# Optimization experiments

Hardware: AMD Instinct MI355X
Metric: run time of the kernel (lower is better)

## Reference

```python
import jax, jax.numpy as jnp
import numpy as np

# ---- model hyperparameters (match init_kwargs) ----
THRESHOLD = 1.0
DECAY = 0.9
RESET = 0.0
BATCH = 256
INPUT_DIM = 1024
HIDDEN_DIM = 2048
OUTPUT_DIM = 10
NUM_LAYERS = 2
SIM_STEPS = 100
SPIKE_PROB = 0.2  # density of input spike bins


def setup_inputs() -> dict:
    key = jax.random.key(0)
    k1, k2, k3, k4 = jax.random.split(key, 4)
    # binary spike bins: [B, input_dim, T]
    input_bins = (jax.random.uniform(k1, (BATCH, INPUT_DIM, SIM_STEPS)) < SPIKE_PROB).astype(jnp.float32)
    W_ih = jax.random.normal(k2, (INPUT_DIM, HIDDEN_DIM), dtype=jnp.float32) * 0.1
    W_hh = jax.random.normal(k3, (NUM_LAYERS - 1, HIDDEN_DIM, HIDDEN_DIM), dtype=jnp.float32) * 0.1
    W_ho = jax.random.normal(k4, (HIDDEN_DIM, OUTPUT_DIM), dtype=jnp.float32) * 0.1
    return {"input_bins": input_bins, "W_ih": W_ih, "W_hh": W_hh, "W_ho": W_ho}


def _lif_step(v, current):
    """One leaky-integrate-and-fire update. v, current: [B, N]."""
    v = v * DECAY + current
    spiked = v >= THRESHOLD
    spikes = jnp.where(spiked, 1.0, 0.0).astype(v.dtype)
    v = jnp.where(spiked, RESET, v)
    return v, spikes


def reference(input_bins, W_ih, W_hh, W_ho):
    B = input_bins.shape[0]
    T = input_bins.shape[2]
    x = jnp.transpose(input_bins, (2, 0, 1))  # [T, B, input_dim]
    v_hidden = tuple(jnp.zeros((B, W_ih.shape[1]), input_bins.dtype) for _ in range(NUM_LAYERS))
    v_out = jnp.zeros((B, W_ho.shape[1]), input_bins.dtype)

    def step(carry, inp_t):
        vs, vo = carry
        vs = list(vs)
        vs[0], s = _lif_step(vs[0], inp_t @ W_ih)
        for i in range(NUM_LAYERS - 1):
            vs[i + 1], s = _lif_step(vs[i + 1], s @ W_hh[i])
        # modulator signal is 0 here -> output_input * (1 + 0*0.1) = output_input
        vo, s_out = _lif_step(vo, s @ W_ho)
        return (tuple(vs), vo), s_out

    _, out_spikes = jax.lax.scan(step, (v_hidden, v_out), x)  # [T, B, output_dim]
    output_rates = out_spikes.sum(axis=0) / T  # [B, output_dim]
    return output_rates
```

## Files before the change

kernel.cpp:

```cpp
#include <hip/hip_runtime.h>
#include <hip/hip_bf16.h>


#define B 256
#define IN_DIM 1024
#define HID 2048
#define OUT_DIM 10
#define T_STEPS 100
#define NCH 4
#define RT (T_STEPS * B)

typedef unsigned long long ull;
typedef int v4i __attribute__((ext_vector_type(4)));

template<int K>
__global__ __launch_bounds__(256) void cvt_w_i8(
    const float* __restrict__ W, signed char* __restrict__ Bq)
{
    constexpr int WPR = K / 64;
    size_t id = (size_t)blockIdx.x * 256 + threadIdx.x;
    if (id >= (size_t)(K / 4) * HID) return;
    int n  = (int)(id % HID);
    int kg = (int)(id / HID);
    int k0 = kg * 4;
    signed char dig[4][4];
#pragma unroll
    for (int i = 0; i < 4; ++i) {
        double w = (double)W[(size_t)(k0 + i) * HID + n];
        long long V = __double2ll_rn(w * 2147483648.0);
#pragma unroll
        for (int c = 0; c < 3; ++c) {
            int r = (int)(signed char)(V & 0xFF);
            dig[c][i] = (signed char)r;
            V = (V - r) >> 8;
        }
        dig[3][i] = (signed char)V;
    }
    int wb = k0 >> 6, lk = (k0 >> 4) & 3, jj = k0 & 15;
    int nb32 = n >> 5, ct = (n >> 4) & 1, li = n & 15;
    int lane = lk * 16 + li;
    size_t base = ((size_t)nb32 * WPR + wb) * 8192 + (size_t)lane * 16 + jj;
#pragma unroll
    for (int c = 0; c < 4; ++c) {
        int pc = (c < 3) ? (c * 2 + ct) : (6 + ct);
        unsigned pk = (unsigned)(unsigned char)dig[c][0]
                    | ((unsigned)(unsigned char)dig[c][1] << 8)
                    | ((unsigned)(unsigned char)dig[c][2] << 16)
                    | ((unsigned)(unsigned char)dig[c][3] << 24);
        *reinterpret_cast<unsigned*>(Bq + base + (size_t)pc * 1024) = pk;
    }
}

__global__ __launch_bounds__(256) void cvt_who(
    const float* __restrict__ who, double* __restrict__ Who64)
{
    int i = blockIdx.x * 256 + threadIdx.x;
    if (i < HID * OUT_DIM) Who64[i] = (double)who[i];
}

__global__ __launch_bounds__(256) void bitpack_input(
    const float* __restrict__ inp, ull* __restrict__ XbitsT)
{
    int g = blockIdx.x * 4 + (threadIdx.x >> 6);
    int lane = threadIdx.x & 63;
    int b = g >> 4;
    int ig = g & 15;
    int i = ig * 64 + lane;
    const float4* p = (const float4*)(inp + ((size_t)b * IN_DIM + i) * T_STEPS);
    ull* dst = XbitsT + (size_t)ig * RT + b;
#pragma unroll 1
    for (int t4 = 0; t4 < T_STEPS / 4; ++t4) {
        float4 v = p[t4];
        ull m0 = __ballot(v.x > 0.5f);
        ull m1 = __ballot(v.y > 0.5f);
        ull m2 = __ballot(v.z > 0.5f);
        ull m3 = __ballot(v.w > 0.5f);
        if (lane == 0) {
            dst[(size_t)(t4 * 4 + 0) * B] = m0;
            dst[(size_t)(t4 * 4 + 1) * B] = m1;
            dst[(size_t)(t4 * 4 + 2) * B] = m2;
            dst[(size_t)(t4 * 4 + 3) * B] = m3;
        }
    }
}

template<int K>
__global__ __launch_bounds__(256, 3) void gemm_i8(
    const ull* __restrict__ bitsT, int row_base,
    const signed char* __restrict__ Bq, float* __restrict__ C)
{
    constexpr int WPR = K / 64;
    constexpr int NP  = WPR / 2;
    __shared__ __align__(16) signed char blds[6][8192];

    const int tid = threadIdx.x;
    const int lane = tid & 63;
    const int wv = __builtin_amdgcn_readfirstlane(tid >> 6);
    const int row0 = blockIdx.x * 128;
    const int c0 = blockIdx.y * 32;
    const int li = lane & 15;
    const int lk = lane >> 4;
    const int sh = lk * 16;
    const int r0l = wv * 32;

    const signed char* __restrict__ bsrc = Bq + (size_t)blockIdx.y * WPR * 8192;
    const ull* __restrict__ m0p = bitsT + (row_base + row0 + r0l + li);
    const ull* __restrict__ m1p = m0p + 16;

    auto stage_b = [&](int w, int slot) {
        const signed char* src = bsrc + (size_t)w * 8192 + lane * 16;
        signed char* db = &blds[0][0] + slot * 8192;
        __builtin_amdgcn_global_load_lds(
            (const __attribute__((address_space(1))) unsigned int*)(src + wv * 1024),
            (__attribute__((address_space(3))) unsigned int*)(db + wv * 1024), 16, 0, 0);
        __builtin_amdgcn_global_load_lds(
            (const __attribute__((address_space(1))) unsigned int*)(src + (wv + 4) * 1024),
            (__attribute__((address_space(3))) unsigned int*)(db + (wv + 4) * 1024), 16, 0, 0);
    };

    stage_b(0, 0);
    stage_b(1, 1);
    stage_b(2, 2);
    stage_b(3, 3);
    ull r0[4], r1[4];
#pragma unroll
    for (int u = 0; u < 4; ++u) {
        r0[u] = m0p[(size_t)u * RT];
        r1[u] = m1p[(size_t)u * RT];
    }
    __syncthreads();

    v4i acc[2][2][NCH];
#pragma unroll
    for (int g = 0; g < 2; ++g)
#pragma unroll
        for (int t = 0; t < 2; ++t)
#pragma unroll
            for (int c = 0; c < NCH; ++c) acc[g][t][c] = (v4i){0, 0, 0, 0};

    int s0 = 0;
#pragma unroll 1
    for (int p2 = 0; p2 < NP; p2 += 2) {
#pragma unroll
        for (int pp = 0; pp < 2; ++pp) {
            const int w0 = (p2 + pp) * 2;
            const int u0 = w0 & 3, u1 = (w0 + 1) & 3;
            int s1 = s0 + 1; if (s1 >= 6) s1 -= 6;
            int t0 = s0 + 4; if (t0 >= 6) t0 -= 6;
            int t1 = s0 + 5; if (t1 >= 6) t1 -= 6;

            int wn0 = w0 + 4; if (wn0 >= WPR) wn0 -= WPR;
            int wn1 = w0 + 5; if (wn1 >= WPR) wn1 -= WPR;
            stage_b(wn0, t0);
            stage_b(wn1, t1);
            ull m00 = r0[u0], m01 = r1[u0];
            ull m10 = r0[u1], m11 = r1[u1];
            r0[u0] = m0p[(size_t)wn0 * RT];
            r1[u0] = m1p[(size_t)wn0 * RT];
            r0[u1] = m0p[(size_t)wn1 * RT];
            r1[u1] = m1p[(size_t)wn1 * RT];

            {
                unsigned sa = (unsigned)(m00 >> sh) & 0xFFFFu;
                unsigned sb = (unsigned)(m01 >> sh) & 0xFFFFu;
                v4i a0, a1;
#pragma unroll
                for (int d = 0; d < 4; ++d) {
                    a0[d] = (int)((((sa >> (4 * d)) & 0xFu) * 0x00204081u) & 0x01010101u);
                    a1[d] = (int)((((sb >> (4 * d)) & 0xFu) * 0x00204081u) & 0x01010101u);
                }
                const signed char* bb = &blds[0][0] + s0 * 8192 + lane * 16;
                __builtin_amdgcn_s_setprio(1);
#pragma unroll
                for (int c = 0; c < NCH; ++c) {
#pragma unroll
                    for (int t = 0; t < 2; ++t) {
                        v4i b = *(const v4i*)(bb + (c * 2 + t) * 1024);
                        acc[0][t][c] = __builtin_amdgcn_mfma_i32_16x16x64_i8(a0, b, acc[0][t][c], 0, 0, 0);
                        acc[1][t][c] = __builtin_amdgcn_mfma_i32_16x16x64_i8(a1, b, acc[1][t][c], 0, 0, 0);
                    }
                }
                __builtin_amdgcn_s_setprio(0);
            }
            {
                unsigned sa = (unsigned)(m10 >> sh) & 0xFFFFu;
                unsigned sb = (unsigned)(m11 >> sh) & 0xFFFFu;
                v4i a0, a1;
#pragma unroll
                for (int d = 0; d < 4; ++d) {
                    a0[d] = (int)((((sa >> (4 * d)) & 0xFu) * 0x00204081u) & 0x01010101u);
                    a1[d] = (int)((((sb >> (4 * d)) & 0xFu) * 0x00204081u) & 0x01010101u);
                }
                const signed char* bb = &blds[0][0] + s1 * 8192 + lane * 16;
                __builtin_amdgcn_s_setprio(1);
#pragma unroll
                for (int c = 0; c < NCH; ++c) {
#pragma unroll
                    for (int t = 0; t < 2; ++t) {
                        v4i b = *(const v4i*)(bb + (c * 2 + t) * 1024);
                        acc[0][t][c] = __builtin_amdgcn_mfma_i32_16x16x64_i8(a0, b, acc[0][t][c], 0, 0, 0);
                        acc[1][t][c] = __builtin_amdgcn_mfma_i32_16x16x64_i8(a1, b, acc[1][t][c], 0, 0, 0);
                    }
                }
                __builtin_amdgcn_s_setprio(0);
            }

            __asm__ __volatile__("s_waitcnt vmcnt(8)\n\ts_barrier" ::: "memory");
            s0 += 2; if (s0 >= 6) s0 -= 6;
        }
    }

#pragma unroll
    for (int g = 0; g < 2; ++g) {
#pragma unroll
        for (int t = 0; t < 2; ++t) {
#pragma unroll
            for (int r = 0; r < 4; ++r) {
                long long V = (long long)acc[g][t][3][r];
                V = (V << 8) + (long long)acc[g][t][2][r];
                V = (V << 8) + (long long)acc[g][t][1][r];
                V = (V << 8) + (long long)acc[g][t][0][r];
                C[(size_t)(row0 + r0l + g * 16 + lk * 4 + r) * HID + c0 + t * 16 + li] =
                    (float)((double)V * 0x1p-31);
            }
        }
    }
}

__global__ __launch_bounds__(256) void gemm_out(
    const ull* __restrict__ bitsT, int row_base,
    const double* __restrict__ W, double* __restrict__ C3)
{
    __shared__ double part[3][64][OUT_DIM];
    const int lane = threadIdx.x & 63;
    const int sl = threadIdx.x >> 6;
    const int row = blockIdx.x * 64 + lane;

    double acc[OUT_DIM];
#pragma unroll
    for (int j = 0; j < OUT_DIM; ++j) acc[j] = 0.0;

    for (int w = sl * 8; w < sl * 8 + 8; ++w) {
        ull m = bitsT[(size_t)w * RT + row_base + row];
        const double* __restrict__ wk = W + (size_t)(w * 64) * OUT_DIM;
#pragma unroll 4
        for (int kk = 0; kk < 64; ++kk) {
            double bd = (double)(unsigned int)(m & 1ull);
            m >>= 1;
#pragma unroll
            for (int j = 0; j < OUT_DIM; ++j)
                acc[j] = fma(bd, wk[j], acc[j]);
            wk += OUT_DIM;
        }
    }
    if (sl) {
#pragma unroll
        for (int j = 0; j < OUT_DIM; ++j) part[sl - 1][lane][j] = acc[j];
    }
    __syncthreads();
    if (sl == 0) {
        double* __restrict__ crow = C3 + (size_t)row * OUT_DIM;
#pragma unroll
        for (int j = 0; j < OUT_DIM; ++j)
            crow[j] = acc[j] + part[0][lane][j] + part[1][lane][j] + part[2][lane][j];
    }
}

__global__ __launch_bounds__(256) void lif_scan(
    const float* __restrict__ C, double* __restrict__ vstate,
    ull* __restrict__ SbitsT, int row_base, int Tl, int first)
{
    int g = blockIdx.x * 4 + (threadIdx.x >> 6);
    int lane = threadIdx.x & 63;
    int b = g >> 5;
    int ng = g & 31;
    int n = ng * 64 + lane;
    const float* __restrict__ Cp = C + (size_t)b * HID + n;
    ull* __restrict__ Sp = SbitsT + (size_t)ng * RT + row_base + b;
    double v = first ? 0.0 : vstate[(size_t)b * HID + n];
    int tl = 0;
    for (; tl + 4 <= Tl; tl += 4) {
        float c0 = Cp[(size_t)(tl + 0) * (B * HID)];
        float c1 = Cp[(size_t)(tl + 1) * (B * HID)];
        float c2 = Cp[(size_t)(tl + 2) * (B * HID)];
        float c3 = Cp[(size_t)(tl + 3) * (B * HID)];
#pragma unroll
        for (int i = 0; i < 4; ++i) {
            float cc = (i == 0) ? c0 : (i == 1) ? c1 : (i == 2) ? c2 : c3;
            v = v * 0.9 + (double)cc;
            bool s = (v >= 1.0);
            if (s) v = 0.0;
            ull mask = __ballot(s);
            if (lane == 0) Sp[(size_t)(tl + i) * B] = mask;
        }
    }
    for (; tl < Tl; ++tl) {
        double c = (double)Cp[(size_t)tl * (B * HID)];
        v = v * 0.9 + c;
        bool s = (v >= 1.0);
        if (s) v = 0.0;
        ull mask = __ballot(s);
        if (lane == 0) Sp[(size_t)tl * B] = mask;
    }
    vstate[(size_t)b * HID + n] = v;
}

__global__ __launch_bounds__(256) void lif_out(
    const double* __restrict__ C3, double* __restrict__ vstate,
    int* __restrict__ cnt_state, float* __restrict__ out, int Tl, int first)
{
    int tid = blockIdx.x * 256 + threadIdx.x;
    if (tid >= B * OUT_DIM) return;
    int b = tid / OUT_DIM, o = tid % OUT_DIM;
    const double* __restrict__ Cp = C3 + (size_t)b * OUT_DIM + o;
    double v = first ? 0.0 : vstate[tid];
    int cnt = first ? 0 : cnt_state[tid];
    int tl = 0;
    for (; tl + 4 <= Tl; tl += 4) {
        double c0 = Cp[(size_t)(tl + 0) * (B * OUT_DIM)];
        double c1 = Cp[(size_t)(tl + 1) * (B * OUT_DIM)];
        double c2 = Cp[(size_t)(tl + 2) * (B * OUT_DIM)];
        double c3 = Cp[(size_t)(tl + 3) * (B * OUT_DIM)];
#pragma unroll
        for (int i = 0; i < 4; ++i) {
            double cc = (i == 0) ? c0 : (i == 1) ? c1 : (i == 2) ? c2 : c3;
            v = v * 0.9 + cc;
            if (v >= 1.0) { cnt++; v = 0.0; }
        }
    }
    for (; tl < Tl; ++tl) {
        double c = Cp[(size_t)tl * (B * OUT_DIM)];
        v = v * 0.9 + c;
        if (v >= 1.0) { cnt++; v = 0.0; }
    }
    vstate[tid] = v;
    cnt_state[tid] = cnt;
    out[tid] = (float)((double)cnt / (double)T_STEPS);
}

extern "C" void kernel_launch(void* const* d_in, const int* in_sizes, int n_in,
                              void* d_out, int out_size, void* d_ws, size_t ws_size,
                              hipStream_t stream) {
    const float* inp = (const float*)d_in[0];
    const float* wih = (const float*)d_in[1];
    const float* whh = (const float*)d_in[2];
    const float* who = (const float*)d_in[3];
    float* out = (float*)d_out;

    unsigned char* p = (unsigned char*)d_ws;
    auto alloc = [&](size_t sz) -> void* {
        void* r = (void*)p;
        p += (sz + 255) & ~(size_t)255;
        return r;
    };
    signed char* Bq1 = (signed char*)alloc((size_t)NCH * HID * IN_DIM + 4096);
    signed char* Bq2 = (signed char*)alloc((size_t)NCH * HID * HID + 4096);
    double* Who64 = (double*)alloc((size_t)HID * OUT_DIM * 8);
    ull* XbitsT = (ull*)alloc((size_t)16 * RT * 8);
    ull* S1T    = (ull*)alloc((size_t)32 * RT * 8);
    ull* S2T    = (ull*)alloc((size_t)32 * RT * 8);
    double* v1 = (double*)alloc((size_t)B * HID * 8);
    double* v2 = (double*)alloc((size_t)B * HID * 8);
    double* vo = (double*)alloc((size_t)B * OUT_DIM * 8);
    int* cnts  = (int*)alloc((size_t)B * OUT_DIM * 4);

    size_t used = (size_t)(p - (unsigned char*)d_ws);
    size_t remain = (ws_size > used) ? (ws_size - used) : 0;
    size_t per_t = (size_t)B * HID * 4 + (size_t)B * OUT_DIM * 8 + 1024;
    int CH = (int)(remain / per_t);
    if (CH > T_STEPS) CH = T_STEPS;
    if (CH < 1) CH = 1;
    double* C3 = (double*)alloc((size_t)CH * B * OUT_DIM * 8);
    float* C   = (float*)alloc((size_t)CH * B * HID * 4);

    cvt_w_i8<IN_DIM><<<((IN_DIM / 4) * HID + 255) / 256, 256, 0, stream>>>(wih, Bq1);
    cvt_w_i8<HID><<<((HID / 4) * HID + 255) / 256, 256, 0, stream>>>(whh, Bq2);
    cvt_who<<<(HID * OUT_DIM + 255) / 256, 256, 0, stream>>>(who, Who64);
    bitpack_input<<<(B * (IN_DIM / 64)) / 4, 256, 0, stream>>>(inp, XbitsT);

    for (int t0 = 0; t0 < T_STEPS; t0 += CH) {
        int L = T_STEPS - t0;
        if (L > CH) L = CH;
        int rows = L * B;
        int first = (t0 == 0) ? 1 : 0;

        gemm_i8<IN_DIM><<<dim3(rows / 128, HID / 32), 256, 0, stream>>>(
            XbitsT, t0 * B, Bq1, C);
        lif_scan<<<(B * (HID / 64)) / 4, 256, 0, stream>>>(
            C, v1, S1T, t0 * B, L, first);

        gemm_i8<HID><<<dim3(rows / 128, HID / 32), 256, 0, stream>>>(
            S1T, t0 * B, Bq2, C);
        lif_scan<<<(B * (HID / 64)) / 4, 256, 0, stream>>>(
            C, v2, S2T, t0 * B, L, first);

        gemm_out<<<rows / 64, 256, 0, stream>>>(S2T, t0 * B, Who64, C3);
        lif_out<<<(B * OUT_DIM + 255) / 256, 256, 0, stream>>>(
            C3, vo, cnts, out, L, first);
    }
}
```

Baseline: 999.0 us.

## Move output projection to int8 MFMA and stage input bitpacking through LDS

Replaces the fp64 FMA loop in the output-layer GEMM with int8 MFMA over 4 byte-planes of fixed-point weights, using a new weight-conversion kernel. The input bitpacking kernel now loads through shared memory in coalesced chunks instead of strided float4 reads per lane. The gemm_i8 wait count changes from 8 to 12, and the weight-plane layout formula is simplified. The changes aim to cut the scalar fp64 cost and uncoalesced input loads. They rely on the same fixed-point decomposition for exactness, and the looser vmcnt could affect the pipeline's correctness margin.

```diff
diff --git a/kernel.cpp b/kernel.cpp
--- a/kernel.cpp
+++ b/kernel.cpp
@@ -42,7 +42,7 @@
     size_t base = ((size_t)nb32 * WPR + wb) * 8192 + (size_t)lane * 16 + jj;
 #pragma unroll
     for (int c = 0; c < 4; ++c) {
-        int pc = (c < 3) ? (c * 2 + ct) : (6 + ct);
+        int pc = c * 2 + ct;
         unsigned pk = (unsigned)(unsigned char)dig[c][0]
                     | ((unsigned)(unsigned char)dig[c][1] << 8)
                     | ((unsigned)(unsigned char)dig[c][2] << 16)
@@ -51,36 +51,79 @@
     }
 }
 
-__global__ __launch_bounds__(256) void cvt_who(
-    const float* __restrict__ who, double* __restrict__ Who64)
-{
-    int i = blockIdx.x * 256 + threadIdx.x;
-    if (i < HID * OUT_DIM) Who64[i] = (double)who[i];
+__global__ __launch_bounds__(256) void cvt_who_i8(
+    const float* __restrict__ who, signed char* __restrict__ Bq3)
+{
+    int id = blockIdx.x * 256 + threadIdx.x;
+    if (id >= 32 * 64 * 4) return;
+    int jg = id & 3;
+    int lane = (id >> 2) & 63;
+    int w = id >> 8;
+    int li = lane & 15, lk = lane >> 4;
+    signed char dig[4][4];
+#pragma unroll
+    for (int i = 0; i < 4; ++i) {
+        int jj = jg * 4 + i;
+        int k = w * 64 + lk * 16 + jj;
+        double x = (li < OUT_DIM) ? (double)who[(size_t)k * OUT_DIM + li] : 0.0;
+        long long V = __double2ll_rn(x * 2147483648.0);
+#pragma unroll
+        for (int c = 0; c < 3; ++c) {
+            int r = (int)(signed char)(V & 0xFF);
+            dig[c][i] = (signed char)r;
+            V = (V - r) >> 8;
+        }
+        dig[3][i] = (signed char)V;
+    }
+    size_t base = (size_t)w * 4096 + (size_t)lane * 16 + jg * 4;
+#pragma unroll
+    for (int c = 0; c < 4; ++c) {
+        unsigned pk = (unsigned)(unsigned char)dig[c][0]
+                    | ((unsigned)(unsigned char)dig[c][1] << 8)
+                    | ((unsigned)(unsigned char)dig[c][2] << 16)
+                    | ((unsigned)(unsigned char)dig[c][3] << 24);
+        *reinterpret_cast<unsigned*>(Bq3 + base + (size_t)c * 1024) = pk;
+    }
 }
 
 __global__ __launch_bounds__(256) void bitpack_input(
     const float* __restrict__ inp, ull* __restrict__ XbitsT)
 {
-    int g = blockIdx.x * 4 + (threadIdx.x >> 6);
-    int lane = threadIdx.x & 63;
-    int b = g >> 4;
-    int ig = g & 15;
-    int i = ig * 64 + lane;
-    const float4* p = (const float4*)(inp + ((size_t)b * IN_DIM + i) * T_STEPS);
-    ull* dst = XbitsT + (size_t)ig * RT + b;
-#pragma unroll 1
-    for (int t4 = 0; t4 < T_STEPS / 4; ++t4) {
-        float4 v = p[t4];
-        ull m0 = __ballot(v.x > 0.5f);
-        ull m1 = __ballot(v.y > 0.5f);
-        ull m2 = __ballot(v.z > 0.5f);
-        ull m3 = __ballot(v.w > 0.5f);
-        if (lane == 0) {
-            dst[(size_t)(t4 * 4 + 0) * B] = m0;
-            dst[(size_t)(t4 * 4 + 1) * B] = m1;
-            dst[(size_t)(t4 * 4 + 2) * B] = m2;
-            dst[(size_t)(t4 * 4 + 3) * B] = m3;
-        }
+    __shared__ float sb[4][64][33];
+    const int wv = threadIdx.x >> 6;
+    const int lane = threadIdx.x & 63;
+    const int g = blockIdx.x * 4 + wv;
+    const int b = g >> 4;
+    const int ig = g & 15;
+    const float* __restrict__ src = inp + ((size_t)b * IN_DIM + ig * 64) * T_STEPS;
+    ull* __restrict__ dst = XbitsT + (size_t)ig * RT + b;
+
+#pragma unroll
+    for (int tc = 0; tc < 4; ++tc) {
+        const int t0 = tc * 32;
+        if (tc < 3) {
+#pragma unroll
+            for (int f4 = 0; f4 < 32; ++f4) {
+                int f = f4 * 64 + lane;
+                int ii = f >> 5, tt = f & 31;
+                sb[wv][ii][tt] = src[ii * T_STEPS + t0 + tt];
+            }
+        } else {
+#pragma unroll
+            for (int f4 = 0; f4 < 4; ++f4) {
+                int f = f4 * 64 + lane;
+                int ii = f >> 2, tt = f & 3;
+                sb[wv][ii][tt] = src[ii * T_STEPS + t0 + tt];
+            }
+        }
+        __syncthreads();
+        const int len = (tc < 3) ? 32 : 4;
+        for (int tt = 0; tt < len; ++tt) {
+            float v = sb[wv][lane][tt];
+            ull m = __ballot(v > 0.5f);
+            if (lane == 0) dst[(size_t)(t0 + tt) * B] = m;
+        }
+        __syncthreads();
     }
 }
 
@@ -205,7 +248,7 @@
                 __builtin_amdgcn_s_setprio(0);
             }
 
-            __asm__ __volatile__("s_waitcnt vmcnt(8)\n\ts_barrier" ::: "memory");
+            __asm__ __volatile__("s_waitcnt vmcnt(12)\n\ts_barrier" ::: "memory");
             s0 += 2; if (s0 >= 6) s0 -= 6;
         }
     }
@@ -229,40 +272,57 @@
 
 __global__ __launch_bounds__(256) void gemm_out(
     const ull* __restrict__ bitsT, int row_base,
-    const double* __restrict__ W, double* __restrict__ C3)
-{
-    __shared__ double part[3][64][OUT_DIM];
+    const signed char* __restrict__ Bq3, double* __restrict__ C3)
+{
     const int lane = threadIdx.x & 63;
-    const int sl = threadIdx.x >> 6;
-    const int row = blockIdx.x * 64 + lane;
-
-    double acc[OUT_DIM];
-#pragma unroll
-    for (int j = 0; j < OUT_DIM; ++j) acc[j] = 0.0;
-
-    for (int w = sl * 8; w < sl * 8 + 8; ++w) {
-        ull m = bitsT[(size_t)w * RT + row_base + row];
-        const double* __restrict__ wk = W + (size_t)(w * 64) * OUT_DIM;
-#pragma unroll 4
-        for (int kk = 0; kk < 64; ++kk) {
-            double bd = (double)(unsigned int)(m & 1ull);
-            m >>= 1;
-#pragma unroll
-            for (int j = 0; j < OUT_DIM; ++j)
-                acc[j] = fma(bd, wk[j], acc[j]);
-            wk += OUT_DIM;
-        }
-    }
-    if (sl) {
-#pragma unroll
-        for (int j = 0; j < OUT_DIM; ++j) part[sl - 1][lane][j] = acc[j];
-    }
-    __syncthreads();
-    if (sl == 0) {
-        double* __restrict__ crow = C3 + (size_t)row * OUT_DIM;
-#pragma unroll
-        for (int j = 0; j < OUT_DIM; ++j)
-            crow[j] = acc[j] + part[0][lane][j] + part[1][lane][j] + part[2][lane][j];
+    const int wv = threadIdx.x >> 6;
+    const int li = lane & 15;
+    const int lk = lane >> 4;
+    const int sh = lk * 16;
+    const int row0 = blockIdx.x * 256 + wv * 64;
+    const ull* __restrict__ mp = bitsT + (row_base + row0 + li);
+
+    v4i acc[4][NCH];
+#pragma unroll
+    for (int g = 0; g < 4; ++g)
+#pragma unroll
+        for (int c = 0; c < NCH; ++c) acc[g][c] = (v4i){0, 0, 0, 0};
+
+#pragma unroll 1
+    for (int w = 0; w < 32; ++w) {
+        ull m[4];
+#pragma unroll
+        for (int g = 0; g < 4; ++g) m[g] = mp[(size_t)w * RT + g * 16];
+        const v4i* __restrict__ bp = (const v4i*)(Bq3 + (size_t)w * 4096 + (size_t)lane * 16);
+        v4i b[NCH];
+#pragma unroll
+        for (int c = 0; c < NCH; ++c) b[c] = bp[c * 64];
+#pragma unroll
+        for (int g = 0; g < 4; ++g) {
+            unsigned s = (unsigned)(m[g] >> sh) & 0xFFFFu;
+            v4i a;
+#pragma unroll
+            for (int d = 0; d < 4; ++d)
+                a[d] = (int)((((s >> (4 * d)) & 0xFu) * 0x00204081u) & 0x01010101u);
+#pragma unroll
+            for (int c = 0; c < NCH; ++c)
+                acc[g][c] = __builtin_amdgcn_mfma_i32_16x16x64_i8(a, b[c], acc[g][c], 0, 0, 0);
+        }
+    }
+
+    if (li < OUT_DIM) {
+#pragma unroll
+        for (int g = 0; g < 4; ++g) {
+#pragma unroll
+            for (int rr = 0; rr < 4; ++rr) {
+                long long V = (long long)acc[g][3][rr];
+                V = (V << 8) + (long long)acc[g][2][rr];
+                V = (V << 8) + (long long)acc[g][1][rr];
+                V = (V << 8) + (long long)acc[g][0][rr];
+                C3[(size_t)(row0 + g * 16 + lk * 4 + rr) * OUT_DIM + li] =
+                    (double)V * 0x1p-31;
+            }
+        }
     }
 }
 
@@ -355,7 +415,7 @@
     };
     signed char* Bq1 = (signed char*)alloc((size_t)NCH * HID * IN_DIM + 4096);
     signed char* Bq2 = (signed char*)alloc((size_t)NCH * HID * HID + 4096);
-    double* Who64 = (double*)alloc((size_t)HID * OUT_DIM * 8);
+    signed char* Bq3 = (signed char*)alloc((size_t)32 * 4096 + 4096);
     ull* XbitsT = (ull*)alloc((size_t)16 * RT * 8);
     ull* S1T    = (ull*)alloc((size_t)32 * RT * 8);
     ull* S2T    = (ull*)alloc((size_t)32 * RT * 8);
@@ -375,7 +435,7 @@
 
     cvt_w_i8<IN_DIM><<<((IN_DIM / 4) * HID + 255) / 256, 256, 0, stream>>>(wih, Bq1);
     cvt_w_i8<HID><<<((HID / 4) * HID + 255) / 256, 256, 0, stream>>>(whh, Bq2);
-    cvt_who<<<(HID * OUT_DIM + 255) / 256, 256, 0, stream>>>(who, Who64);
+    cvt_who_i8<<<32, 256, 0, stream>>>(who, Bq3);
     bitpack_input<<<(B * (IN_DIM / 64)) / 4, 256, 0, stream>>>(inp, XbitsT);
 
     for (int t0 = 0; t0 < T_STEPS; t0 += CH) {
@@ -394,7 +454,7 @@
         lif_scan<<<(B * (HID / 64)) / 4, 256, 0, stream>>>(
             C, v2, S2T, t0 * B, L, first);
 
-        gemm_out<<<rows / 64, 256, 0, stream>>>(S2T, t0 * B, Who64, C3);
+        gemm_out<<<rows / 256, 256, 0, stream>>>(S2T, t0 * B, Bq3, C3);
         lif_out<<<(B * OUT_DIM + 255) / 256, 256, 0, stream>>>(
             C3, vo, cnts, out, L, first);
     }
```

Result: faster. 859.1 us (-14.0%).
